# Optimization experiments

Measured on AMD Instinct MI355X. Metric: run time of the kernel, lower is better.

## Reference

```python
import jax, jax.numpy as jnp
import numpy as np

B, T, D, H = 64, 512, 1024, 1024


def setup_inputs() -> dict:
    key = jax.random.key(0)
    ks = jax.random.split(key, 6)
    std = 1.0 / np.sqrt(H)  # torch reset_parameters: uniform(-std, std)
    x = jax.random.normal(ks[0], (B, T, D), dtype=jnp.float32)
    teacher_mask = jax.random.uniform(ks[1], (B, T), dtype=jnp.float32)
    Wx = jax.random.uniform(ks[2], (4 * H, D), minval=-std, maxval=std, dtype=jnp.float32)
    bx = jax.random.uniform(ks[3], (4 * H,), minval=-std, maxval=std, dtype=jnp.float32)
    Wh = jax.random.uniform(ks[4], (4 * H, H), minval=-std, maxval=std, dtype=jnp.float32)
    bh = jax.random.uniform(ks[5], (4 * H,), minval=-std, maxval=std, dtype=jnp.float32)
    return {"x": x, "teacher_mask": teacher_mask, "Wx": Wx, "bx": bx, "Wh": Wh, "bh": bh}


def reference(x, teacher_mask, Wx, bx, Wh, bh):
    b = x.shape[0]
    h0 = jnp.zeros((b, H), dtype=x.dtype)
    c0 = jnp.zeros((b, H), dtype=x.dtype)
    xs = jnp.swapaxes(x, 0, 1)                      # [T, B, D]
    ms = jnp.swapaxes(teacher_mask, 0, 1)[..., None]  # [T, B, 1]

    def step(carry, inp):
        hn, cn = carry
        x_t, m = inp
        # teacher_fn(seq, (hn, cn), x_t) := hn (previous hidden); blend with mask
        new_x = m * hn + (1.0 - m) * x_t
        gates = new_x @ Wx.T + bx + hn @ Wh.T + bh   # [B, 4H]
        i, f, g, o = jnp.split(gates, 4, axis=1)     # torch chunk order: i, f, g, o
        i = jax.nn.sigmoid(i)
        f = jax.nn.sigmoid(f)
        g = jnp.tanh(g)
        o = jax.nn.sigmoid(o)
        cy = cn * f + i * g
        hy = o * jnp.tanh(cy)
        return (hy, cy), hy

    (hn, cn), ys = jax.lax.scan(step, (h0, c0), (xs, ms))
    out = jnp.swapaxes(ys, 0, 1)                     # [B, T, H]
    return out, hn, cn
```

## Files before the change

kernel.cpp:

```cpp
#include <hip/hip_runtime.h>
#include <stdint.h>


#define B_ 64
#define T_ 512
#define D_ 1024
#define H_ 1024
#define NBLK 256
#define UPB 8
#define NROW 32
#define NTHR 512

typedef __attribute__((ext_vector_type(8))) short short8;
typedef __attribute__((ext_vector_type(16))) float f32x16;

#define WH_OFF 65536
#define GBUF_OFF 131072
#define MLDS_OFF 147968
#define BIAS_OFF 148480
#define SMEM_BYTES 148608

#define WS_MT 4096
#define WS_HBUF 135168
#define WS_XP 397312
#define HSLOT 65536

__device__ __forceinline__ unsigned f2bf(float f) {
  unsigned u = __float_as_uint(f);
  return (u + 0x7FFFu + ((u >> 16) & 1u)) >> 16;
}
__device__ __forceinline__ float sigf(float x) { return 1.0f / (1.0f + __expf(-x)); }
__device__ __forceinline__ float tanhf_(float x) { return 1.0f - 2.0f / (__expf(2.0f * x) + 1.0f); }

__global__ void prep_m(const float* __restrict__ tm, float* __restrict__ mT) {
  int i = blockIdx.x * blockDim.x + threadIdx.x;
  if (i >= B_ * T_) return;
  int b = i >> 9, t = i & (T_ - 1);
  mT[t * B_ + b] = tm[i];
}

__global__ void prep_x(const float* __restrict__ x, unsigned short* __restrict__ xp) {
  int i = blockIdx.x * blockDim.x + threadIdx.x;
  if (i >= B_ * T_ * D_ / 8) return;
  const int dblk = i & 127, t = (i >> 7) & (T_ - 1), b = i >> 16;
  const float* src = x + ((size_t)b * T_ + t) * D_ + dblk * 8;
  float4 a0 = *(const float4*)src;
  float4 a1 = *(const float4*)(src + 4);
  short8 r;
  r[0] = (short)f2bf(a0.x); r[1] = (short)f2bf(a0.y);
  r[2] = (short)f2bf(a0.z); r[3] = (short)f2bf(a0.w);
  r[4] = (short)f2bf(a1.x); r[5] = (short)f2bf(a1.y);
  r[6] = (short)f2bf(a1.z); r[7] = (short)f2bf(a1.w);
  *(short8*)(xp + ((size_t)(t * 128 + dblk) * 64 + b) * 8) = r;
}

template<int XB>
__global__ __launch_bounds__(NTHR, 1)
void lstm_persist(const float* __restrict__ xf,
                  const unsigned short* __restrict__ xp,
                  const float* __restrict__ mT,
                  const float* __restrict__ Wx, const float* __restrict__ bxp,
                  const float* __restrict__ Wh, const float* __restrict__ bhp,
                  float* __restrict__ out,
                  unsigned short* __restrict__ hbuf,
                  unsigned* __restrict__ flags,
                  unsigned* __restrict__ gen)
{
  extern __shared__ char smem[];
  float* gbuf     = (float*)(smem + GBUF_OFF);
  float* m_lds    = (float*)(smem + MLDS_OFF);
  float* bias_lds = (float*)(smem + BIAS_OFF);

  const int tid = threadIdx.x;
  const int bid = blockIdx.x;
  const int ug  = bid >> 1;
  const int bg  = bid & 1;

  for (int i = 0; i < 32; ++i) {
    const int s  = i * NTHR + tid;
    const int dw = s & 3, n = (s >> 2) & 31, kgs = (s >> 7) & 1;
    const int js = (s >> 8) & 7, kos = s >> 11;
    const int grow = (n >> 3) * H_ + ug * UPB + (n & 7);
    const int k = kos * 128 + js * 16 + kgs * 8 + dw * 2;
    const unsigned byte = (unsigned)(kos * 8192 + js * 1024 + kgs * 512 + n * 16 + dw * 4);
    float2 v = *(const float2*)(Wx + (size_t)grow * D_ + k);
    *(unsigned*)(smem + byte) = f2bf(v.x) | (f2bf(v.y) << 16);
    v = *(const float2*)(Wh + (size_t)grow * H_ + k);
    *(unsigned*)(smem + WH_OFF + byte) = f2bf(v.x) | (f2bf(v.y) << 16);
  }
  if (tid < NROW) {
    const int grow = (tid >> 3) * H_ + ug * UPB + (tid & 7);
    bias_lds[tid] = bxp[grow] + bhp[grow];
  }

  const int lane = tid & 63;
  const int wid  = tid >> 6;
  const int ko   = wid;
  const int l31  = lane & 31;
  const int kg   = lane >> 5;
  const int b0   = bg * 32;

  const unsigned wxbase = (unsigned)(ko * 8192 + kg * 512 + l31 * 16);
#define LWX(J) (*(const short8*)(smem + wxbase + (unsigned)((J) * 1024)))
#define LWH(J) (*(const short8*)(smem + WH_OFF + wxbase + (unsigned)((J) * 1024)))
  const size_t hull0 = ((size_t)(ko * 16 + kg) * 64 + (b0 + l31)) * 2;
  const size_t xsh0 = ((size_t)(ko * 16 + kg) * 64 + (b0 + l31)) * 8;

  const int act = (tid < 256);
  const int cb2 = (tid >> 3) & 31;
  const int cu  = tid & 7;
  const int b   = b0 + cb2;
  const int hu  = ug * UPB + cu;
  float ccell = 0.0f, hv = 0.0f;

  __syncthreads();

  f32x16 accX = {0,0,0,0,0,0,0,0,0,0,0,0,0,0,0,0};
  if (XB) {
    const unsigned short* xb = xp + xsh0;
#pragma unroll
    for (int j = 0; j < 8; ++j)
      accX = __builtin_amdgcn_mfma_f32_32x32x16_bf16(
          *(const short8*)(xb + j * 1024), LWX(j), accX, 0, 0, 0);
  } else {
    const float* xsrc = xf + (size_t)(b0 + l31) * T_ * D_ + ko * 128 + kg * 8;
#pragma unroll
    for (int j = 0; j < 8; ++j) {
      float4 a0 = *(const float4*)(xsrc + j * 16);
      float4 a1 = *(const float4*)(xsrc + j * 16 + 4);
      short8 r;
      r[0] = (short)f2bf(a0.x); r[1] = (short)f2bf(a0.y);
      r[2] = (short)f2bf(a0.z); r[3] = (short)f2bf(a0.w);
      r[4] = (short)f2bf(a1.x); r[5] = (short)f2bf(a1.y);
      r[6] = (short)f2bf(a1.z); r[7] = (short)f2bf(a1.w);
      accX = __builtin_amdgcn_mfma_f32_32x32x16_bf16(r, LWX(j), accX, 0, 0, 0);
    }
  }
  if (tid < B_) m_lds[tid] = mT[tid];
  __syncthreads();

  for (int t = 0; t < T_; ++t) {
    const int nxt = (t + 1 < T_) ? (t + 1) : t;
    const unsigned tgt = (unsigned)(t + 1);

    const unsigned long long* hp =
        (const unsigned long long*)(hbuf + (size_t)(t & 1) * HSLOT) + hull0;
    short8 hf[8];
#pragma unroll
    for (int j = 0; j < 8; ++j) {
      unsigned long long lo = __hip_atomic_load(hp + (size_t)j * 256,
                                                __ATOMIC_RELAXED, __HIP_MEMORY_SCOPE_AGENT);
      unsigned long long hi = __hip_atomic_load(hp + (size_t)j * 256 + 1,
                                                __ATOMIC_RELAXED, __HIP_MEMORY_SCOPE_AGENT);
      ((unsigned long long*)&hf[j])[0] = lo;
      ((unsigned long long*)&hf[j])[1] = hi;
    }
    f32x16 accA = {0,0,0,0,0,0,0,0,0,0,0,0,0,0,0,0};
    f32x16 accC = {0,0,0,0,0,0,0,0,0,0,0,0,0,0,0,0};
#pragma unroll
    for (int j = 0; j < 8; ++j) {
      accA = __builtin_amdgcn_mfma_f32_32x32x16_bf16(hf[j], LWX(j), accA, 0, 0, 0);
      accC = __builtin_amdgcn_mfma_f32_32x32x16_bf16(hf[j], LWH(j), accC, 0, 0, 0);
    }

    const float* ml = m_lds + (t & 1) * B_;
    const int s = wid & 3;
    if (wid < 4) {
#pragma unroll
      for (int e = 0; e < 16; ++e) {
        const int br = (e & 3) + 8 * (e >> 2) + 4 * kg;
        const float mv = ml[b0 + br];
        float g = mv * accA[e] + (1.0f - mv) * accX[e] + accC[e];
        if (wid == 0) g += bias_lds[l31];
        gbuf[(s * 32 + br) * 33 + l31] = g;
      }
    }
    __syncthreads();
    if (wid >= 4) {
#pragma unroll
      for (int e = 0; e < 16; ++e) {
        const int br = (e & 3) + 8 * (e >> 2) + 4 * kg;
        const float mv = ml[b0 + br];
        gbuf[(s * 32 + br) * 33 + l31] += mv * accA[e] + (1.0f - mv) * accX[e] + accC[e];
      }
    }
    __syncthreads();

    if (act) {
      float gi = 0.0f, gf = 0.0f, gg = 0.0f, go = 0.0f;
#pragma unroll
      for (int sl = 0; sl < 4; ++sl) {
        const float* row = gbuf + (sl * 32 + cb2) * 33;
        gi += row[cu];      gf += row[8 + cu];
        gg += row[16 + cu]; go += row[24 + cu];
      }
      const float iv = sigf(gi), fv = sigf(gf), gv = tanhf_(gg), ov = sigf(go);
      ccell = ccell * fv + iv * gv;
      hv = ov * tanhf_(ccell);
      __hip_atomic_store(hbuf + (size_t)((t + 1) & 1) * HSLOT +
                             ((hu >> 3) * 64 + b) * 8 + (hu & 7),
                         (unsigned short)f2bf(hv),
                         __ATOMIC_RELAXED, __HIP_MEMORY_SCOPE_AGENT);
    }

    __syncthreads();

    if (bid == 0) {
      if (wid == 0) {
        for (;;) {
          unsigned v0 = (lane == 0) ? tgt
              : __hip_atomic_load(flags + lane, __ATOMIC_RELAXED, __HIP_MEMORY_SCOPE_AGENT);
          unsigned v1 = __hip_atomic_load(flags + 64 + lane,
                                          __ATOMIC_RELAXED, __HIP_MEMORY_SCOPE_AGENT);
          unsigned v2 = __hip_atomic_load(flags + 128 + lane,
                                          __ATOMIC_RELAXED, __HIP_MEMORY_SCOPE_AGENT);
          unsigned v3 = __hip_atomic_load(flags + 192 + lane,
                                          __ATOMIC_RELAXED, __HIP_MEMORY_SCOPE_AGENT);
          if (__all((v0 >= tgt) && (v1 >= tgt) && (v2 >= tgt) && (v3 >= tgt))) break;
          __builtin_amdgcn_s_sleep(1);
        }
        if (lane == 0)
          __hip_atomic_store(gen, tgt, __ATOMIC_RELAXED, __HIP_MEMORY_SCOPE_AGENT);
      }
    } else {
      if (tid == 0)
        __hip_atomic_store(flags + bid, tgt,
                           __ATOMIC_RELAXED, __HIP_MEMORY_SCOPE_AGENT);
    }

    if (act) out[((size_t)b * T_ + t) * H_ + hu] = hv;
    f32x16 accXn = {0,0,0,0,0,0,0,0,0,0,0,0,0,0,0,0};
    if (XB) {
      const unsigned short* xb = xp + (size_t)nxt * (128 * 64 * 8) + xsh0;
#pragma unroll
      for (int j = 0; j < 8; ++j)
        accXn = __builtin_amdgcn_mfma_f32_32x32x16_bf16(
            *(const short8*)(xb + j * 1024), LWX(j), accXn, 0, 0, 0);
    } else {
      const float* xsrc = xf + ((size_t)(b0 + l31) * T_ + nxt) * D_ + ko * 128 + kg * 8;
#pragma unroll
      for (int j = 0; j < 8; ++j) {
        float4 a0 = *(const float4*)(xsrc + j * 16);
        float4 a1 = *(const float4*)(xsrc + j * 16 + 4);
        short8 r;
        r[0] = (short)f2bf(a0.x); r[1] = (short)f2bf(a0.y);
        r[2] = (short)f2bf(a0.z); r[3] = (short)f2bf(a0.w);
        r[4] = (short)f2bf(a1.x); r[5] = (short)f2bf(a1.y);
        r[6] = (short)f2bf(a1.z); r[7] = (short)f2bf(a1.w);
        accXn = __builtin_amdgcn_mfma_f32_32x32x16_bf16(r, LWX(j), accXn, 0, 0, 0);
      }
    }
    if (tid < B_) m_lds[((t + 1) & 1) * B_ + tid] = mT[nxt * B_ + tid];

    if (bid != 0 && wid == 0) {
      while (__hip_atomic_load(gen, __ATOMIC_RELAXED, __HIP_MEMORY_SCOPE_AGENT) < tgt)
        __builtin_amdgcn_s_sleep(1);
    }
    __syncthreads();
    __builtin_amdgcn_sched_barrier(0);

    accX = accXn;
  }

  if (act) {
    out[(size_t)B_ * T_ * H_ + (size_t)b * H_ + hu] = hv;
    out[(size_t)B_ * T_ * H_ + (size_t)B_ * H_ + (size_t)b * H_ + hu] = ccell;
  }
}

extern "C" void kernel_launch(void* const* d_in, const int* in_sizes, int n_in,
                              void* d_out, int out_size, void* d_ws, size_t ws_size,
                              hipStream_t stream) {
  const float* x  = (const float*)d_in[0];
  const float* tm = (const float*)d_in[1];
  const float* Wx = (const float*)d_in[2];
  const float* bx = (const float*)d_in[3];
  const float* Wh = (const float*)d_in[4];
  const float* bh = (const float*)d_in[5];
  float* out = (float*)d_out;
  char* ws = (char*)d_ws;

  unsigned* flags      = (unsigned*)ws;
  unsigned* gen        = (unsigned*)(ws + 2048);
  float* mT            = (float*)(ws + WS_MT);
  unsigned short* hbuf = (unsigned short*)(ws + WS_HBUF);
  unsigned short* xp   = (unsigned short*)(ws + WS_XP);

  const size_t need_xp = (size_t)WS_XP + 2ull * B_ * T_ * D_;
  const bool use_xp = ws_size >= need_xp;

  hipMemsetAsync(ws, 0, WS_HBUF + 2 * HSLOT * 2, stream);
  prep_m<<<dim3((B_ * T_ + 255) / 256), dim3(256), 0, stream>>>(tm, mT);
  if (use_xp) {
    const int n = B_ * T_ * D_ / 8;
    prep_x<<<dim3((n + 255) / 256), dim3(256), 0, stream>>>(x, xp);
    lstm_persist<1><<<dim3(NBLK), dim3(NTHR), SMEM_BYTES, stream>>>(
        x, xp, mT, Wx, bx, Wh, bh, out, hbuf, flags, gen);
  } else {
    lstm_persist<0><<<dim3(NBLK), dim3(NTHR), SMEM_BYTES, stream>>>(
        x, xp, mT, Wx, bx, Wh, bh, out, hbuf, flags, gen);
  }
}
```

Baseline: 2.827 ms.

## Split grid barrier into per-batch-half domains with a dedicated sync wavefront

The two batch halves never exchange hidden state, so the single 256-block grid barrier is replaced by two independent 128-block barriers. Each has its own flag array and generation counter, with blocks 0 and 1 acting as masters. A ninth wavefront is added to each block to do the flag signalling and spinning. This lets the next step's input-projection MFMAs and output stores in the other eight waves overlap with barrier polling. The cost is one more wave per block and a few more `wid < 8` guards; the per-step barrier latency and serialization on a single master should shrink.

```diff
diff --git a/kernel.cpp b/kernel.cpp
--- a/kernel.cpp
+++ b/kernel.cpp
@@ -9,7 +9,7 @@
 #define NBLK 256
 #define UPB 8
 #define NROW 32
-#define NTHR 512
+#define BTHR 576
 
 typedef __attribute__((ext_vector_type(8))) short short8;
 typedef __attribute__((ext_vector_type(16))) float f32x16;
@@ -55,7 +55,7 @@
 }
 
 template<int XB>
-__global__ __launch_bounds__(NTHR, 1)
+__global__ __launch_bounds__(BTHR, 1)
 void lstm_persist(const float* __restrict__ xf,
                   const unsigned short* __restrict__ xp,
                   const float* __restrict__ mT,
@@ -76,17 +76,19 @@
   const int ug  = bid >> 1;
   const int bg  = bid & 1;
 
-  for (int i = 0; i < 32; ++i) {
-    const int s  = i * NTHR + tid;
-    const int dw = s & 3, n = (s >> 2) & 31, kgs = (s >> 7) & 1;
-    const int js = (s >> 8) & 7, kos = s >> 11;
-    const int grow = (n >> 3) * H_ + ug * UPB + (n & 7);
-    const int k = kos * 128 + js * 16 + kgs * 8 + dw * 2;
-    const unsigned byte = (unsigned)(kos * 8192 + js * 1024 + kgs * 512 + n * 16 + dw * 4);
-    float2 v = *(const float2*)(Wx + (size_t)grow * D_ + k);
-    *(unsigned*)(smem + byte) = f2bf(v.x) | (f2bf(v.y) << 16);
-    v = *(const float2*)(Wh + (size_t)grow * H_ + k);
-    *(unsigned*)(smem + WH_OFF + byte) = f2bf(v.x) | (f2bf(v.y) << 16);
+  if (tid < 512) {
+    for (int i = 0; i < 32; ++i) {
+      const int s  = i * 512 + tid;
+      const int dw = s & 3, n = (s >> 2) & 31, kgs = (s >> 7) & 1;
+      const int js = (s >> 8) & 7, kos = s >> 11;
+      const int grow = (n >> 3) * H_ + ug * UPB + (n & 7);
+      const int k = kos * 128 + js * 16 + kgs * 8 + dw * 2;
+      const unsigned byte = (unsigned)(kos * 8192 + js * 1024 + kgs * 512 + n * 16 + dw * 4);
+      float2 v = *(const float2*)(Wx + (size_t)grow * D_ + k);
+      *(unsigned*)(smem + byte) = f2bf(v.x) | (f2bf(v.y) << 16);
+      v = *(const float2*)(Wh + (size_t)grow * H_ + k);
+      *(unsigned*)(smem + WH_OFF + byte) = f2bf(v.x) | (f2bf(v.y) << 16);
+    }
   }
   if (tid < NROW) {
     const int grow = (tid >> 3) * H_ + ug * UPB + (tid & 7);
@@ -95,7 +97,7 @@
 
   const int lane = tid & 63;
   const int wid  = tid >> 6;
-  const int ko   = wid;
+  const int ko   = wid & 7;
   const int l31  = lane & 31;
   const int kg   = lane >> 5;
   const int b0   = bg * 32;
@@ -104,140 +106,29 @@
 #define LWX(J) (*(const short8*)(smem + wxbase + (unsigned)((J) * 1024)))
 #define LWH(J) (*(const short8*)(smem + WH_OFF + wxbase + (unsigned)((J) * 1024)))
   const size_t hull0 = ((size_t)(ko * 16 + kg) * 64 + (b0 + l31)) * 2;
-  const size_t xsh0 = ((size_t)(ko * 16 + kg) * 64 + (b0 + l31)) * 8;
+  const size_t xsh0  = ((size_t)(ko * 16 + kg) * 64 + (b0 + l31)) * 8;
 
   const int act = (tid < 256);
   const int cb2 = (tid >> 3) & 31;
   const int cu  = tid & 7;
   const int b   = b0 + cb2;
   const int hu  = ug * UPB + cu;
+  unsigned* dom_flags = flags + (bg << 7);
+  unsigned* dom_gen   = gen + bg * 32;
   float ccell = 0.0f, hv = 0.0f;
 
   __syncthreads();
 
   f32x16 accX = {0,0,0,0,0,0,0,0,0,0,0,0,0,0,0,0};
-  if (XB) {
-    const unsigned short* xb = xp + xsh0;
-#pragma unroll
-    for (int j = 0; j < 8; ++j)
-      accX = __builtin_amdgcn_mfma_f32_32x32x16_bf16(
-          *(const short8*)(xb + j * 1024), LWX(j), accX, 0, 0, 0);
-  } else {
-    const float* xsrc = xf + (size_t)(b0 + l31) * T_ * D_ + ko * 128 + kg * 8;
-#pragma unroll
-    for (int j = 0; j < 8; ++j) {
-      float4 a0 = *(const float4*)(xsrc + j * 16);
-      float4 a1 = *(const float4*)(xsrc + j * 16 + 4);
-      short8 r;
-      r[0] = (short)f2bf(a0.x); r[1] = (short)f2bf(a0.y);
-      r[2] = (short)f2bf(a0.z); r[3] = (short)f2bf(a0.w);
-      r[4] = (short)f2bf(a1.x); r[5] = (short)f2bf(a1.y);
-      r[6] = (short)f2bf(a1.z); r[7] = (short)f2bf(a1.w);
-      accX = __builtin_amdgcn_mfma_f32_32x32x16_bf16(r, LWX(j), accX, 0, 0, 0);
-    }
-  }
-  if (tid < B_) m_lds[tid] = mT[tid];
-  __syncthreads();
-
-  for (int t = 0; t < T_; ++t) {
-    const int nxt = (t + 1 < T_) ? (t + 1) : t;
-    const unsigned tgt = (unsigned)(t + 1);
-
-    const unsigned long long* hp =
-        (const unsigned long long*)(hbuf + (size_t)(t & 1) * HSLOT) + hull0;
-    short8 hf[8];
-#pragma unroll
-    for (int j = 0; j < 8; ++j) {
-      unsigned long long lo = __hip_atomic_load(hp + (size_t)j * 256,
-                                                __ATOMIC_RELAXED, __HIP_MEMORY_SCOPE_AGENT);
-      unsigned long long hi = __hip_atomic_load(hp + (size_t)j * 256 + 1,
-                                                __ATOMIC_RELAXED, __HIP_MEMORY_SCOPE_AGENT);
-      ((unsigned long long*)&hf[j])[0] = lo;
-      ((unsigned long long*)&hf[j])[1] = hi;
-    }
-    f32x16 accA = {0,0,0,0,0,0,0,0,0,0,0,0,0,0,0,0};
-    f32x16 accC = {0,0,0,0,0,0,0,0,0,0,0,0,0,0,0,0};
-#pragma unroll
-    for (int j = 0; j < 8; ++j) {
-      accA = __builtin_amdgcn_mfma_f32_32x32x16_bf16(hf[j], LWX(j), accA, 0, 0, 0);
-      accC = __builtin_amdgcn_mfma_f32_32x32x16_bf16(hf[j], LWH(j), accC, 0, 0, 0);
-    }
-
-    const float* ml = m_lds + (t & 1) * B_;
-    const int s = wid & 3;
-    if (wid < 4) {
-#pragma unroll
-      for (int e = 0; e < 16; ++e) {
-        const int br = (e & 3) + 8 * (e >> 2) + 4 * kg;
-        const float mv = ml[b0 + br];
-        float g = mv * accA[e] + (1.0f - mv) * accX[e] + accC[e];
-        if (wid == 0) g += bias_lds[l31];
-        gbuf[(s * 32 + br) * 33 + l31] = g;
-      }
-    }
-    __syncthreads();
-    if (wid >= 4) {
-#pragma unroll
-      for (int e = 0; e < 16; ++e) {
-        const int br = (e & 3) + 8 * (e >> 2) + 4 * kg;
-        const float mv = ml[b0 + br];
-        gbuf[(s * 32 + br) * 33 + l31] += mv * accA[e] + (1.0f - mv) * accX[e] + accC[e];
-      }
-    }
-    __syncthreads();
-
-    if (act) {
-      float gi = 0.0f, gf = 0.0f, gg = 0.0f, go = 0.0f;
-#pragma unroll
-      for (int sl = 0; sl < 4; ++sl) {
-        const float* row = gbuf + (sl * 32 + cb2) * 33;
-        gi += row[cu];      gf += row[8 + cu];
-        gg += row[16 + cu]; go += row[24 + cu];
-      }
-      const float iv = sigf(gi), fv = sigf(gf), gv = tanhf_(gg), ov = sigf(go);
-      ccell = ccell * fv + iv * gv;
-      hv = ov * tanhf_(ccell);
-      __hip_atomic_store(hbuf + (size_t)((t + 1) & 1) * HSLOT +
-                             ((hu >> 3) * 64 + b) * 8 + (hu & 7),
-                         (unsigned short)f2bf(hv),
-                         __ATOMIC_RELAXED, __HIP_MEMORY_SCOPE_AGENT);
-    }
-
-    __syncthreads();
-
-    if (bid == 0) {
-      if (wid == 0) {
-        for (;;) {
-          unsigned v0 = (lane == 0) ? tgt
-              : __hip_atomic_load(flags + lane, __ATOMIC_RELAXED, __HIP_MEMORY_SCOPE_AGENT);
-          unsigned v1 = __hip_atomic_load(flags + 64 + lane,
-                                          __ATOMIC_RELAXED, __HIP_MEMORY_SCOPE_AGENT);
-          unsigned v2 = __hip_atomic_load(flags + 128 + lane,
-                                          __ATOMIC_RELAXED, __HIP_MEMORY_SCOPE_AGENT);
-          unsigned v3 = __hip_atomic_load(flags + 192 + lane,
-                                          __ATOMIC_RELAXED, __HIP_MEMORY_SCOPE_AGENT);
-          if (__all((v0 >= tgt) && (v1 >= tgt) && (v2 >= tgt) && (v3 >= tgt))) break;
-          __builtin_amdgcn_s_sleep(1);
-        }
-        if (lane == 0)
-          __hip_atomic_store(gen, tgt, __ATOMIC_RELAXED, __HIP_MEMORY_SCOPE_AGENT);
-      }
+  if (wid < 8) {
+    if (XB) {
+      const unsigned short* xb = xp + xsh0;
+#pragma unroll
+      for (int j = 0; j < 8; ++j)
+        accX = __builtin_amdgcn_mfma_f32_32x32x16_bf16(
+            *(const short8*)(xb + j * 1024), LWX(j), accX, 0, 0, 0);
     } else {
-      if (tid == 0)
-        __hip_atomic_store(flags + bid, tgt,
-                           __ATOMIC_RELAXED, __HIP_MEMORY_SCOPE_AGENT);
-    }
-
-    if (act) out[((size_t)b * T_ + t) * H_ + hu] = hv;
-    f32x16 accXn = {0,0,0,0,0,0,0,0,0,0,0,0,0,0,0,0};
-    if (XB) {
-      const unsigned short* xb = xp + (size_t)nxt * (128 * 64 * 8) + xsh0;
-#pragma unroll
-      for (int j = 0; j < 8; ++j)
-        accXn = __builtin_amdgcn_mfma_f32_32x32x16_bf16(
-            *(const short8*)(xb + j * 1024), LWX(j), accXn, 0, 0, 0);
-    } else {
-      const float* xsrc = xf + ((size_t)(b0 + l31) * T_ + nxt) * D_ + ko * 128 + kg * 8;
+      const float* xsrc = xf + (size_t)(b0 + l31) * T_ * D_ + ko * 128 + kg * 8;
 #pragma unroll
       for (int j = 0; j < 8; ++j) {
         float4 a0 = *(const float4*)(xsrc + j * 16);
@@ -247,18 +138,128 @@
         r[2] = (short)f2bf(a0.z); r[3] = (short)f2bf(a0.w);
         r[4] = (short)f2bf(a1.x); r[5] = (short)f2bf(a1.y);
         r[6] = (short)f2bf(a1.z); r[7] = (short)f2bf(a1.w);
-        accXn = __builtin_amdgcn_mfma_f32_32x32x16_bf16(r, LWX(j), accXn, 0, 0, 0);
+        accX = __builtin_amdgcn_mfma_f32_32x32x16_bf16(r, LWX(j), accX, 0, 0, 0);
+      }
+    }
+  }
+  if (tid < B_) m_lds[tid] = mT[tid];
+  __syncthreads();
+
+  for (int t = 0; t < T_; ++t) {
+    const int nxt = (t + 1 < T_) ? (t + 1) : t;
+    const unsigned tgt = (unsigned)(t + 1);
+
+    f32x16 accA = {0,0,0,0,0,0,0,0,0,0,0,0,0,0,0,0};
+    f32x16 accC = {0,0,0,0,0,0,0,0,0,0,0,0,0,0,0,0};
+    if (wid < 8) {
+      const unsigned long long* hp =
+          (const unsigned long long*)(hbuf + (size_t)(t & 1) * HSLOT) + hull0;
+      short8 hf[8];
+#pragma unroll
+      for (int j = 0; j < 8; ++j) {
+        unsigned long long lo = __hip_atomic_load(hp + (size_t)j * 256,
+                                                  __ATOMIC_RELAXED, __HIP_MEMORY_SCOPE_AGENT);
+        unsigned long long hi = __hip_atomic_load(hp + (size_t)j * 256 + 1,
+                                                  __ATOMIC_RELAXED, __HIP_MEMORY_SCOPE_AGENT);
+        ((unsigned long long*)&hf[j])[0] = lo;
+        ((unsigned long long*)&hf[j])[1] = hi;
+      }
+#pragma unroll
+      for (int j = 0; j < 8; ++j) {
+        accA = __builtin_amdgcn_mfma_f32_32x32x16_bf16(hf[j], LWX(j), accA, 0, 0, 0);
+        accC = __builtin_amdgcn_mfma_f32_32x32x16_bf16(hf[j], LWH(j), accC, 0, 0, 0);
+      }
+    }
+
+    const float* ml = m_lds + (t & 1) * B_;
+    const int s = wid & 3;
+    if (wid < 4) {
+#pragma unroll
+      for (int e = 0; e < 16; ++e) {
+        const int br = (e & 3) + 8 * (e >> 2) + 4 * kg;
+        const float mv = ml[b0 + br];
+        float g = mv * accA[e] + (1.0f - mv) * accX[e] + accC[e];
+        if (wid == 0) g += bias_lds[l31];
+        gbuf[(s * 32 + br) * 33 + l31] = g;
+      }
+    }
+    __syncthreads();
+    if (wid >= 4 && wid < 8) {
+#pragma unroll
+      for (int e = 0; e < 16; ++e) {
+        const int br = (e & 3) + 8 * (e >> 2) + 4 * kg;
+        const float mv = ml[b0 + br];
+        gbuf[(s * 32 + br) * 33 + l31] += mv * accA[e] + (1.0f - mv) * accX[e] + accC[e];
+      }
+    }
+    __syncthreads();
+
+    if (act) {
+      float gi = 0.0f, gf = 0.0f, gg = 0.0f, go = 0.0f;
+#pragma unroll
+      for (int sl = 0; sl < 4; ++sl) {
+        const float* row = gbuf + (sl * 32 + cb2) * 33;
+        gi += row[cu];      gf += row[8 + cu];
+        gg += row[16 + cu]; go += row[24 + cu];
+      }
+      const float iv = sigf(gi), fv = sigf(gf), gv = tanhf_(gg), ov = sigf(go);
+      ccell = ccell * fv + iv * gv;
+      hv = ov * tanhf_(ccell);
+      __hip_atomic_store(hbuf + (size_t)((t + 1) & 1) * HSLOT +
+                             ((hu >> 3) * 64 + b) * 8 + (hu & 7),
+                         (unsigned short)f2bf(hv),
+                         __ATOMIC_RELAXED, __HIP_MEMORY_SCOPE_AGENT);
+    }
+
+    __syncthreads();
+    if (tid == 0)
+      __hip_atomic_store(dom_flags + ug, tgt,
+                         __ATOMIC_RELAXED, __HIP_MEMORY_SCOPE_AGENT);
+
+    if (wid == 8) {
+      if (bid == bg) {
+        for (;;) {
+          unsigned v0 = __hip_atomic_load(dom_flags + lane,
+                                          __ATOMIC_RELAXED, __HIP_MEMORY_SCOPE_AGENT);
+          unsigned v1 = __hip_atomic_load(dom_flags + 64 + lane,
+                                          __ATOMIC_RELAXED, __HIP_MEMORY_SCOPE_AGENT);
+          if (__all((v0 >= tgt) && (v1 >= tgt))) break;
+          __builtin_amdgcn_s_sleep(1);
+        }
+        if (lane == 0)
+          __hip_atomic_store(dom_gen, tgt, __ATOMIC_RELAXED, __HIP_MEMORY_SCOPE_AGENT);
+      }
+      while (__hip_atomic_load(dom_gen, __ATOMIC_RELAXED, __HIP_MEMORY_SCOPE_AGENT) < tgt)
+        __builtin_amdgcn_s_sleep(1);
+    }
+
+    if (act) out[((size_t)b * T_ + t) * H_ + hu] = hv;
+    f32x16 accXn = {0,0,0,0,0,0,0,0,0,0,0,0,0,0,0,0};
+    if (wid < 8) {
+      if (XB) {
+        const unsigned short* xb = xp + (size_t)nxt * (128 * 64 * 8) + xsh0;
+#pragma unroll
+        for (int j = 0; j < 8; ++j)
+          accXn = __builtin_amdgcn_mfma_f32_32x32x16_bf16(
+              *(const short8*)(xb + j * 1024), LWX(j), accXn, 0, 0, 0);
+      } else {
+        const float* xsrc = xf + ((size_t)(b0 + l31) * T_ + nxt) * D_ + ko * 128 + kg * 8;
+#pragma unroll
+        for (int j = 0; j < 8; ++j) {
+          float4 a0 = *(const float4*)(xsrc + j * 16);
+          float4 a1 = *(const float4*)(xsrc + j * 16 + 4);
+          short8 r;
+          r[0] = (short)f2bf(a0.x); r[1] = (short)f2bf(a0.y);
+          r[2] = (short)f2bf(a0.z); r[3] = (short)f2bf(a0.w);
+          r[4] = (short)f2bf(a1.x); r[5] = (short)f2bf(a1.y);
+          r[6] = (short)f2bf(a1.z); r[7] = (short)f2bf(a1.w);
+          accXn = __builtin_amdgcn_mfma_f32_32x32x16_bf16(r, LWX(j), accXn, 0, 0, 0);
+        }
       }
     }
     if (tid < B_) m_lds[((t + 1) & 1) * B_ + tid] = mT[nxt * B_ + tid];
 
-    if (bid != 0 && wid == 0) {
-      while (__hip_atomic_load(gen, __ATOMIC_RELAXED, __HIP_MEMORY_SCOPE_AGENT) < tgt)
-        __builtin_amdgcn_s_sleep(1);
-    }
     __syncthreads();
-    __builtin_amdgcn_sched_barrier(0);
-
     accX = accXn;
   }
 
@@ -294,10 +295,10 @@
   if (use_xp) {
     const int n = B_ * T_ * D_ / 8;
     prep_x<<<dim3((n + 255) / 256), dim3(256), 0, stream>>>(x, xp);
-    lstm_persist<1><<<dim3(NBLK), dim3(NTHR), SMEM_BYTES, stream>>>(
+    lstm_persist<1><<<dim3(NBLK), dim3(BTHR), SMEM_BYTES, stream>>>(
         x, xp, mT, Wx, bx, Wh, bh, out, hbuf, flags, gen);
   } else {
-    lstm_persist<0><<<dim3(NBLK), dim3(NTHR), SMEM_BYTES, stream>>>(
+    lstm_persist<0><<<dim3(NBLK), dim3(BTHR), SMEM_BYTES, stream>>>(
         x, xp, mT, Wx, bx, Wh, bh, out, hbuf, flags, gen);
   }
 }
```

Result: faster. 2.716 ms (median of 2 runs) (-3.9%).
